# Kernel tuning notes

Hardware: AMD Instinct MI355X
Metric: run time of the kernel (lower is better)

Reference implementation:

```python
import jax, jax.numpy as jnp
import numpy as np


def _rope_tables(N, d, base=10000.0):
    # LLaMA-style: freqs over even dims, interleaved (pairs) layout
    inv = 1.0 / (base ** (np.arange(0, d, 2)[: d // 2].astype(np.float32) / d))
    ang = np.outer(np.arange(N, dtype=np.float32), inv)  # [N, d/2]
    return jnp.asarray(np.cos(ang), jnp.float32), jnp.asarray(np.sin(ang), jnp.float32)


def _apply_rope(x, cos, sin):
    # x: [B, h, N, d]; pairs layout (..., d/2, 2)
    B, h, N, d = x.shape
    xs = x.reshape(B, h, N, d // 2, 2)
    x0, x1 = xs[..., 0], xs[..., 1]
    c = cos[None, None, :, :]
    s = sin[None, None, :, :]
    o0 = x0 * c - x1 * s
    o1 = x1 * c + x0 * s
    return jnp.stack([o0, o1], axis=-1).reshape(B, h, N, d)


def _neighborhood_attn(q, k, v, window, scale):
    # q,k,v: [B, h, H, W, d]; NATTEN-style clamped window of size window x window
    B, h, H, W, d = q.shape
    r = window // 2
    ih = jnp.clip(jnp.arange(H) - r, 0, H - window)[:, None] + jnp.arange(window)  # [H, w]
    iw = jnp.clip(jnp.arange(W) - r, 0, W - window)[:, None] + jnp.arange(window)  # [W, w]
    # gather windows: [B, h, H, W, w, w, d]
    kwin = k[:, :, ih[:, None, :, None], iw[None, :, None, :], :]
    vwin = v[:, :, ih[:, None, :, None], iw[None, :, None, :], :]
    attn = jnp.einsum('bhijd,bhijpqd->bhijpq', q, kwin) * scale
    attn = jax.nn.softmax(attn.reshape(B, h, H, W, window * window), axis=-1)
    out = jnp.einsum('bhijp,bhijpd->bhijd', attn,
                     vwin.reshape(B, h, H, W, window * window, d))
    return out  # [B, h, H, W, d]


def setup_inputs() -> dict:
    key = jax.random.key(0)
    k1, k2, k3 = jax.random.split(key, 3)
    B, H, W, C = 2, 56, 56, 256
    N = H * W
    x = jax.random.normal(k1, (B, N, C), dtype=jnp.float32)
    Wqkv = jax.random.normal(k2, (C, 3 * C), dtype=jnp.float32) * 0.02
    Wproj = jax.random.normal(k3, (C, C), dtype=jnp.float32) * 0.02
    bproj = jnp.zeros((C,), dtype=jnp.float32)
    return {"x": x, "Wqkv": Wqkv, "Wproj": Wproj, "bproj": bproj, "H": H, "W": W}


def reference(x, Wqkv, Wproj, bproj, H, W):
    head_dim = 32
    window = 7
    B, N, C = x.shape
    heads = C // head_dim
    scale = head_dim ** (-0.5)

    qkv = (x @ Wqkv).reshape(B, N, 3, heads, head_dim)
    qkv = jnp.transpose(qkv, (2, 0, 3, 1, 4))  # [3, B, h, N, d]
    q, k, v = qkv[0], qkv[1], qkv[2]

    cos, sin = _rope_tables(N, head_dim)
    q = _apply_rope(q, cos, sin)
    k = _apply_rope(k, cos, sin)

    q = q.reshape(B, heads, H, W, head_dim)
    k = k.reshape(B, heads, H, W, head_dim)
    v = v.reshape(B, heads, H, W, head_dim)

    out = _neighborhood_attn(q, k, v, window, scale)  # [B, h, H, W, d]
    out = out.reshape(B, heads, N, head_dim)
    out = jnp.transpose(out, (0, 2, 1, 3)).reshape(B, N, C)
    return out @ Wproj + bproj
```

## Files before the change

kernel.cpp:

```cpp
#include <hip/hip_runtime.h>
#include <hip/hip_bf16.h>

#define HH 56
#define WW 56
#define NPOS 3136
#define BATCH 2
#define HEADS 8

typedef __attribute__((ext_vector_type(4))) float floatx4;
typedef __attribute__((ext_vector_type(8))) short short8;
typedef __attribute__((ext_vector_type(2))) _Float16 half2v;

static __device__ __forceinline__ ushort f2b(float f) {
    __hip_bfloat16 h = __float2bfloat16(f);
    return *reinterpret_cast<ushort*>(&h);
}
static __device__ __forceinline__ float b2f(ushort u) {
    return __uint_as_float(((uint)u) << 16);
}
static __device__ __forceinline__ ushort f2h(float f) {
    union { _Float16 h; ushort u; } c; c.h = (_Float16)f; return c.u;
}
static __device__ __forceinline__ half2v u2h2(uint u) {
    union { uint u; half2v h; } c; c.u = u; return c.h;
}

static __device__ __forceinline__ void async16(const ushort* g, ushort* l) {
    __builtin_amdgcn_global_load_lds(
        (const __attribute__((address_space(1))) unsigned int*)g,
        (__attribute__((address_space(3))) unsigned int*)l, 16, 0, 0);
}

__constant__ float INVF[16] = {
    1.0f,   0.5623413251903491f,   0.31622776601683794f,   0.17782794100389228f,
    0.1f,   0.05623413251903491f,  0.031622776601683794f,  0.017782794100389228f,
    0.01f,  0.005623413251903491f, 0.0031622776601683794f, 0.0017782794100389228f,
    0.001f, 0.0005623413251903491f,0.00031622776601683794f,0.00017782794100389228f
};

#define QSCALE 0.17677669529663687f


__global__ __launch_bounds__(256) void prep(
    const float* __restrict__ wqkv, const float* __restrict__ wproj,
    ushort* __restrict__ wqkvT, ushort* __restrict__ wprojT)
{
    __shared__ ushort Ls[64 * 65];
    const int bid = blockIdx.x, t = threadIdx.x;
    if (bid < 48) {
        int nb = (bid % 12) * 64, kb = (bid / 12) * 64;
#pragma unroll
        for (int i = 0; i < 16; ++i) {
            int e = t + 256 * i, kk = e >> 6, nn = e & 63;
            Ls[kk * 65 + nn] = f2b(wqkv[(size_t)(kb + kk) * 768 + nb + nn]);
        }
        __syncthreads();
#pragma unroll
        for (int i = 0; i < 16; ++i) {
            int e = t + 256 * i, nn = e >> 6, kk = e & 63;
            wqkvT[(size_t)(nb + nn) * 256 + kb + kk] = Ls[kk * 65 + nn];
        }
    } else {
        int l = bid - 48;
        int nb = (l & 3) * 64, kb = (l >> 2) * 64;
#pragma unroll
        for (int i = 0; i < 16; ++i) {
            int e = t + 256 * i, kk = e >> 6, nn = e & 63;
            Ls[kk * 65 + nn] = f2b(wproj[(size_t)(kb + kk) * 256 + nb + nn]);
        }
        __syncthreads();
#pragma unroll
        for (int i = 0; i < 16; ++i) {
            int e = t + 256 * i, nn = e >> 6, kk = e & 63;
            wprojT[(size_t)(nb + nn) * 256 + kb + kk] = Ls[kk * 65 + nn];
        }
    }
}

__global__ __launch_bounds__(256) void qkv_fast(
    const float* __restrict__ x, const ushort* __restrict__ wqkvT,
    ushort* __restrict__ qb, ushort* __restrict__ kws, ushort* __restrict__ vws)
{
    __shared__ ushort Ab[128 * 32];
    __shared__ ushort Bb[128 * 32];
    const int t = threadIdx.x;
    const int lane = t & 63, wv = t >> 6;
    const int qm = lane & 15, quad = lane >> 4;
    const int m0 = blockIdx.y * 128, n0 = blockIdx.x * 128;
    const int wr = wv >> 1, wc = wv & 1;
    const int srow = lane >> 2, scol = (lane & 3) * 8;
    const int arow = t >> 1, aseg = (t & 1) * 16;

    floatx4 acc[4][4];
#pragma unroll
    for (int i = 0; i < 4; ++i)
#pragma unroll
        for (int j = 0; j < 4; ++j) acc[i][j] = (floatx4){0.f, 0.f, 0.f, 0.f};

    for (int k0 = 0; k0 < 256; k0 += 32) {
#pragma unroll
        for (int i = 0; i < 4; ++i) {
            int col = aseg + i * 4;
            float4 v = *(const float4*)&x[(size_t)(m0 + arow) * 256 + k0 + col];
            ushort4 h; h.x = f2b(v.x); h.y = f2b(v.y); h.z = f2b(v.z); h.w = f2b(v.w);
            *(ushort4*)&Ab[arow * 32 + col] = h;
        }
#pragma unroll
        for (int j = 0; j < 2; ++j) {
            int rbase = wv * 32 + j * 16;
            async16(&wqkvT[(size_t)(n0 + rbase + srow) * 256 + k0 + scol], &Bb[rbase * 32]);
        }
        __syncthreads();
        short8 af[4], bf[4];
#pragma unroll
        for (int mt = 0; mt < 4; ++mt)
            af[mt] = *(const short8*)&Ab[(wr * 64 + mt * 16 + qm) * 32 + quad * 8];
#pragma unroll
        for (int nt = 0; nt < 4; ++nt)
            bf[nt] = *(const short8*)&Bb[(wc * 64 + nt * 16 + qm) * 32 + quad * 8];
#pragma unroll
        for (int mt = 0; mt < 4; ++mt)
#pragma unroll
            for (int nt = 0; nt < 4; ++nt)
                acc[mt][nt] = __builtin_amdgcn_mfma_f32_16x16x32_bf16(af[mt], bf[nt], acc[mt][nt], 0, 0, 0);
        __syncthreads();
    }

    const int whichB = n0 >> 8;
#pragma unroll
    for (int mt = 0; mt < 4; ++mt) {
#pragma unroll
        for (int r = 0; r < 4; ++r) {
            int m = m0 + wr * 64 + mt * 16 + quad * 4 + r;
            int b = (m >= NPOS) ? 1 : 0;
            int pos = m - b * NPOS;
            float c0 = 0.f, s0 = 0.f, c1 = 0.f, s1 = 0.f;
            if (whichB < 2) {
                float posf = (float)pos;
                __sincosf(posf * INVF[qm >> 1], &s0, &c0);
                __sincosf(posf * INVF[8 + (qm >> 1)], &s1, &c1);
            }
#pragma unroll
            for (int nt = 0; nt < 4; ++nt) {
                int c = n0 + wc * 64 + nt * 16 + qm;
                int head = (c >> 5) & 7;
                int d = (nt & 1) * 16 + qm;
                float val = acc[mt][nt][r];
                if (whichB < 2) {
                    float other = __shfl_xor(val, 1);
                    float cf = (nt & 1) ? c1 : c0, sf = (nt & 1) ? s1 : s0;
                    val = (lane & 1) ? (val * cf + other * sf)
                                     : (val * cf - other * sf);
                }
                if (whichB == 0) {
                    qb[(size_t)m * 256 + head * 32 + d] = f2h(val * QSCALE);
                } else {
                    ushort* dst = (whichB == 1) ? kws : vws;
                    dst[(size_t)(((b << 3) + head) * NPOS + pos) * 32 + d] = f2h(val);
                }
            }
        }
    }
}

__global__ __launch_bounds__(256) void nattn(
    const ushort* __restrict__ kws, const ushort* __restrict__ vws,
    const ushort* __restrict__ qb, ushort* __restrict__ ab)
{
    __shared__ ushort Ksm[196 * 32];
    __shared__ ushort Vsm[196 * 32];
    const int t = threadIdx.x;
    const int bh = blockIdx.y;
    const int b = bh >> 3, head = bh & 7;
    const int ti = blockIdx.x / 7, tj = blockIdx.x % 7;
    const int ty0 = ti * 8, tx0 = tj * 8;
    const int r0 = min(max(ty0 - 3, 0), HH - 14);
    const int c0 = min(max(tx0 - 3, 0), WW - 14);
    const ushort* kbase = kws + (size_t)bh * NPOS * 32;
    const ushort* vbase = vws + (size_t)bh * NPOS * 32;

    for (int idx = t; idx < 196 * 4; idx += 256) {
        int p = idx >> 2, ch = idx & 3;
        int g = ((r0 + p / 14) * WW + (c0 + p % 14)) * 32 + ch * 8;
        *(uint4*)&Ksm[p * 32 + ch * 8] = *(const uint4*)&kbase[g];
        *(uint4*)&Vsm[p * 32 + ch * 8] = *(const uint4*)&vbase[g];
    }
    __syncthreads();

    const int lane = t & 63, wv = t >> 6;
    const int qsub = lane & 15, part = lane >> 4;
    const int qi = wv * 16 + qsub;
    const int qy = ty0 + (qi >> 3), qx = tx0 + (qi & 7);
    const int pos = qy * WW + qx;
    const size_t qoff = (size_t)(b * NPOS + pos) * 256 + head * 32;

    half2v qp[16];
    {
        const uint* q4 = (const uint*)(qb + qoff);
#pragma unroll
        for (int c2 = 0; c2 < 16; ++c2) qp[c2] = u2h2(q4[c2]);
    }

    const int rs = min(max(qy - 3, 0), HH - 7) - r0;
    const int cs = min(max(qx - 3, 0), WW - 7) - c0;

    float sum = 0.f;
    float facc[32];
#pragma unroll
    for (int c = 0; c < 32; ++c) facc[c] = 0.f;

#pragma unroll
    for (int j = 0; j < 13; ++j) {
        int kk = part + 4 * j;
        if (kk < 49) {
            int kp = (rs + kk / 7) * 14 + (cs + kk % 7);
            const uint4* Kp = (const uint4*)&Ksm[kp * 32];
            float s = 0.f;
#pragma unroll
            for (int c8 = 0; c8 < 4; ++c8) {
                uint4 u = Kp[c8];
#if __has_builtin(__builtin_amdgcn_fdot2)
                s = __builtin_amdgcn_fdot2(u2h2(u.x), qp[4 * c8 + 0], s, false);
                s = __builtin_amdgcn_fdot2(u2h2(u.y), qp[4 * c8 + 1], s, false);
                s = __builtin_amdgcn_fdot2(u2h2(u.z), qp[4 * c8 + 2], s, false);
                s = __builtin_amdgcn_fdot2(u2h2(u.w), qp[4 * c8 + 3], s, false);
#else
                half2v k0h = u2h2(u.x), k1h = u2h2(u.y), k2h = u2h2(u.z), k3h = u2h2(u.w);
                half2v q0 = qp[4 * c8 + 0], q1 = qp[4 * c8 + 1];
                half2v q2 = qp[4 * c8 + 2], q3 = qp[4 * c8 + 3];
                s += (float)k0h[0] * (float)q0[0] + (float)k0h[1] * (float)q0[1];
                s += (float)k1h[0] * (float)q1[0] + (float)k1h[1] * (float)q1[1];
                s += (float)k2h[0] * (float)q2[0] + (float)k2h[1] * (float)q2[1];
                s += (float)k3h[0] * (float)q3[0] + (float)k3h[1] * (float)q3[1];
#endif
            }
            float e = __expf(s);
            sum += e;
            const uint4* Vp = (const uint4*)&Vsm[kp * 32];
#pragma unroll
            for (int c8 = 0; c8 < 4; ++c8) {
                uint4 u = Vp[c8];
                float* fv = facc + 8 * c8;
                half2v h0 = u2h2(u.x), h1 = u2h2(u.y), h2 = u2h2(u.z), h3 = u2h2(u.w);
                fv[0] += e * (float)h0[0]; fv[1] += e * (float)h0[1];
                fv[2] += e * (float)h1[0]; fv[3] += e * (float)h1[1];
                fv[4] += e * (float)h2[0]; fv[5] += e * (float)h2[1];
                fv[6] += e * (float)h3[0]; fv[7] += e * (float)h3[1];
            }
        }
    }
    sum += __shfl_xor(sum, 16);
    sum += __shfl_xor(sum, 32);
#pragma unroll
    for (int c = 0; c < 32; ++c) {
        facc[c] += __shfl_xor(facc[c], 16);
        facc[c] += __shfl_xor(facc[c], 32);
    }

    if (part == 0) {
        float inv = 1.f / sum;
        uint* op = (uint*)(ab + qoff);
#pragma unroll
        for (int c2 = 0; c2 < 16; ++c2) {
            uint lo = f2b(facc[2 * c2] * inv);
            uint hi = f2b(facc[2 * c2 + 1] * inv);
            op[c2] = lo | (hi << 16);
        }
    }
}

__global__ __launch_bounds__(256) void proj_fast(
    const ushort* __restrict__ ab, const ushort* __restrict__ wprojT,
    const float* __restrict__ bias, float* __restrict__ out)
{
    __shared__ ushort Ap[64 * 32];
    __shared__ ushort Bp[64 * 32];
    const int t = threadIdx.x;
    const int lane = t & 63, wv = t >> 6;
    const int qm = lane & 15, quad = lane >> 4;
    const int n0 = blockIdx.x * 64, m0 = blockIdx.y * 64;
    const int wr = wv >> 1, wc = wv & 1;
    const int srow = lane >> 2, scol = (lane & 3) * 8;

    floatx4 acc[2][2];
#pragma unroll
    for (int i = 0; i < 2; ++i)
#pragma unroll
        for (int j = 0; j < 2; ++j) acc[i][j] = (floatx4){0.f, 0.f, 0.f, 0.f};

    for (int k0 = 0; k0 < 256; k0 += 32) {
        int rbase = wv * 16;
        async16(&ab[(size_t)(m0 + rbase + srow) * 256 + k0 + scol], &Ap[rbase * 32]);
        async16(&wprojT[(size_t)(n0 + rbase + srow) * 256 + k0 + scol], &Bp[rbase * 32]);
        __syncthreads();
        short8 af[2], bf[2];
#pragma unroll
        for (int mt = 0; mt < 2; ++mt)
            af[mt] = *(const short8*)&Ap[(wr * 32 + mt * 16 + qm) * 32 + quad * 8];
#pragma unroll
        for (int nt = 0; nt < 2; ++nt)
            bf[nt] = *(const short8*)&Bp[(wc * 32 + nt * 16 + qm) * 32 + quad * 8];
#pragma unroll
        for (int mt = 0; mt < 2; ++mt)
#pragma unroll
            for (int nt = 0; nt < 2; ++nt)
                acc[mt][nt] = __builtin_amdgcn_mfma_f32_16x16x32_bf16(af[mt], bf[nt], acc[mt][nt], 0, 0, 0);
        __syncthreads();
    }

#pragma unroll
    for (int nt = 0; nt < 2; ++nt) {
        int c = n0 + wc * 32 + nt * 16 + qm;
        float bv = bias[c];
#pragma unroll
        for (int mt = 0; mt < 2; ++mt) {
#pragma unroll
            for (int r = 0; r < 4; ++r) {
                int m = m0 + wr * 32 + mt * 16 + quad * 4 + r;
                out[(size_t)m * 256 + c] = acc[mt][nt][r] + bv;
            }
        }
    }
}

__global__ __launch_bounds__(256) void qkv_fb(
    const float* __restrict__ x, const float* __restrict__ w,
    float* __restrict__ qa, ushort* __restrict__ kws, ushort* __restrict__ vws)
{
    __shared__ ushort Asm[64 * 40];
    __shared__ ushort Bsm[64 * 40];
    const int t = threadIdx.x;
    const int m0 = blockIdx.y * 64;
    const int n0 = blockIdx.x * 64;
    const int lane = t & 63, wv = t >> 6;
    const int qm = lane & 15, quad = lane >> 4;

    floatx4 acc[4];
#pragma unroll
    for (int i = 0; i < 4; ++i) acc[i] = (floatx4){0.f, 0.f, 0.f, 0.f};

    for (int k0 = 0; k0 < 256; k0 += 32) {
#pragma unroll
        for (int i = 0; i < 2; ++i) {
            int p = t + 256 * i;
            int row = p >> 3, f4 = p & 7;
            float4 v = *(const float4*)&x[(size_t)(m0 + row) * 256 + k0 + f4 * 4];
            ushort4 h;
            h.x = f2b(v.x); h.y = f2b(v.y); h.z = f2b(v.z); h.w = f2b(v.w);
            *(ushort4*)&Asm[row * 40 + f4 * 4] = h;
        }
#pragma unroll
        for (int i = 0; i < 8; ++i) {
            int e = t + 256 * i;
            int kk = e >> 6, nn = e & 63;
            Bsm[nn * 40 + kk] = f2b(w[(size_t)(k0 + kk) * 768 + n0 + nn]);
        }
        __syncthreads();
        short8 af = *(const short8*)&Asm[(wv * 16 + qm) * 40 + quad * 8];
#pragma unroll
        for (int nt = 0; nt < 4; ++nt) {
            short8 bf = *(const short8*)&Bsm[(nt * 16 + qm) * 40 + quad * 8];
            acc[nt] = __builtin_amdgcn_mfma_f32_16x16x32_bf16(af, bf, acc[nt], 0, 0, 0);
        }
        __syncthreads();
    }

    const int whichB = n0 >> 8;
#pragma unroll
    for (int r = 0; r < 4; ++r) {
        int m = m0 + wv * 16 + quad * 4 + r;
        int b = (m >= NPOS) ? 1 : 0;
        int pos = m - b * NPOS;
        float cf[2], sf[2];
        if (whichB < 2) {
            float posf = (float)pos;
            __sincosf(posf * INVF[qm >> 1], &sf[0], &cf[0]);
            __sincosf(posf * INVF[8 + (qm >> 1)], &sf[1], &cf[1]);
        }
#pragma unroll
        for (int nt = 0; nt < 4; ++nt) {
            int par = nt & 1;
            int d = par * 16 + qm;
            int head = ((n0 >> 5) & 7) + (nt >> 1);
            float val = acc[nt][r];
            if (whichB < 2) {
                float other = __shfl_xor(val, 1);
                val = (lane & 1) ? (val * cf[par] + other * sf[par])
                                 : (val * cf[par] - other * sf[par]);
            }
            if (whichB == 0) {
                qa[(size_t)m * 256 + head * 32 + d] = val;
            } else {
                ushort* dst = (whichB == 1) ? kws : vws;
                dst[(size_t)(((b << 3) + head) * NPOS + pos) * 32 + d] = f2b(val);
            }
        }
    }
}

__global__ __launch_bounds__(256) void nattn_fb(
    const ushort* __restrict__ kws, const ushort* __restrict__ vws, float* qa)
{
    __shared__ ushort Ksm[196 * 32];
    __shared__ ushort Vsm[196 * 32];
    const int t = threadIdx.x;
    const int bh = blockIdx.y;
    const int b = bh >> 3, head = bh & 7;
    const int ti = blockIdx.x / 7, tj = blockIdx.x % 7;
    const int ty0 = ti * 8, tx0 = tj * 8;
    const int r0 = min(max(ty0 - 3, 0), HH - 14);
    const int c0 = min(max(tx0 - 3, 0), WW - 14);
    const ushort* kbase = kws + (size_t)bh * NPOS * 32;
    const ushort* vbase = vws + (size_t)bh * NPOS * 32;

    for (int idx = t; idx < 196 * 4; idx += 256) {
        int p = idx >> 2, ch = idx & 3;
        int g = ((r0 + p / 14) * WW + (c0 + p % 14)) * 32 + ch * 8;
        *(uint4*)&Ksm[p * 32 + ch * 8] = *(const uint4*)&kbase[g];
        *(uint4*)&Vsm[p * 32 + ch * 8] = *(const uint4*)&vbase[g];
    }
    __syncthreads();

    const int lane = t & 63, wv = t >> 6;
    const int qsub = lane & 15, part = lane >> 4;
    const int qi = wv * 16 + qsub;
    const int qy = ty0 + (qi >> 3), qx = tx0 + (qi & 7);
    const int pos = qy * WW + qx;
    float* qptr = qa + (size_t)(b * NPOS + pos) * 256 + head * 32;

    float qf[32];
#pragma unroll
    for (int c4 = 0; c4 < 8; ++c4) {
        float4 v = *(const float4*)&qptr[c4 * 4];
        qf[4 * c4] = v.x; qf[4 * c4 + 1] = v.y; qf[4 * c4 + 2] = v.z; qf[4 * c4 + 3] = v.w;
    }

    const int rs = min(max(qy - 3, 0), HH - 7) - r0;
    const int cs = min(max(qx - 3, 0), WW - 7) - c0;

    float sum = 0.f;
    float facc[32];
#pragma unroll
    for (int c = 0; c < 32; ++c) facc[c] = 0.f;
#pragma unroll
    for (int j = 0; j < 13; ++j) {
        int kk = part + 4 * j;
        if (kk < 49) {
            int kp = (rs + kk / 7) * 14 + (cs + kk % 7);
            const uint4* Kp = (const uint4*)&Ksm[kp * 32];
            float s = 0.f;
#pragma unroll
            for (int c8 = 0; c8 < 4; ++c8) {
                uint4 u = Kp[c8];
                const float* qv = qf + 8 * c8;
                s += qv[0] * b2f((ushort)u.x) + qv[1] * b2f((ushort)(u.x >> 16));
                s += qv[2] * b2f((ushort)u.y) + qv[3] * b2f((ushort)(u.y >> 16));
                s += qv[4] * b2f((ushort)u.z) + qv[5] * b2f((ushort)(u.z >> 16));
                s += qv[6] * b2f((ushort)u.w) + qv[7] * b2f((ushort)(u.w >> 16));
            }
            float e = __expf(s * 0.17677669529663687f);
            sum += e;
            const uint4* Vp = (const uint4*)&Vsm[kp * 32];
#pragma unroll
            for (int c8 = 0; c8 < 4; ++c8) {
                uint4 u = Vp[c8];
                float* fv = facc + 8 * c8;
                fv[0] += e * b2f((ushort)u.x); fv[1] += e * b2f((ushort)(u.x >> 16));
                fv[2] += e * b2f((ushort)u.y); fv[3] += e * b2f((ushort)(u.y >> 16));
                fv[4] += e * b2f((ushort)u.z); fv[5] += e * b2f((ushort)(u.z >> 16));
                fv[6] += e * b2f((ushort)u.w); fv[7] += e * b2f((ushort)(u.w >> 16));
            }
        }
    }
    sum += __shfl_xor(sum, 16);
    sum += __shfl_xor(sum, 32);
#pragma unroll
    for (int c = 0; c < 32; ++c) {
        facc[c] += __shfl_xor(facc[c], 16);
        facc[c] += __shfl_xor(facc[c], 32);
    }

    if (part == 0) {
        float inv = 1.f / sum;
#pragma unroll
        for (int c4 = 0; c4 < 8; ++c4) {
            float4 o;
            o.x = facc[4 * c4] * inv; o.y = facc[4 * c4 + 1] * inv;
            o.z = facc[4 * c4 + 2] * inv; o.w = facc[4 * c4 + 3] * inv;
            *(float4*)&qptr[c4 * 4] = o;
        }
    }
}

__global__ __launch_bounds__(256) void proj_fb(
    const float* __restrict__ w, const float* __restrict__ bias, float* out)
{
    __shared__ ushort Apad[64 * 264];
    __shared__ ushort Bsm[256 * 40];
    const int t = threadIdx.x;
    const int m0 = blockIdx.x * 64;
    const int lane = t & 63, wv = t >> 6;
    const int qm = lane & 15, quad = lane >> 4;

    {
        int row = t >> 2, cb = (t & 3) * 64;
        const float4* src = (const float4*)&out[(size_t)(m0 + row) * 256 + cb];
#pragma unroll
        for (int i = 0; i < 16; ++i) {
            float4 v = src[i];
            ushort4 h;
            h.x = f2b(v.x); h.y = f2b(v.y); h.z = f2b(v.z); h.w = f2b(v.w);
            *(ushort4*)&Apad[row * 264 + cb + i * 4] = h;
        }
    }

    floatx4 acc[4][4];
#pragma unroll
    for (int i = 0; i < 4; ++i)
#pragma unroll
        for (int j = 0; j < 4; ++j) acc[i][j] = (floatx4){0.f, 0.f, 0.f, 0.f};

    __syncthreads();

    for (int k0 = 0; k0 < 256; k0 += 32) {
#pragma unroll
        for (int i = 0; i < 32; ++i) {
            int e = t + 256 * i;
            int kk = e >> 8, nn = e & 255;
            Bsm[nn * 40 + kk] = f2b(w[(size_t)(k0 + kk) * 256 + nn]);
        }
        __syncthreads();
        short8 af[4];
#pragma unroll
        for (int mt = 0; mt < 4; ++mt)
            af[mt] = *(const short8*)&Apad[(mt * 16 + qm) * 264 + k0 + quad * 8];
#pragma unroll
        for (int nt = 0; nt < 4; ++nt) {
            short8 bf = *(const short8*)&Bsm[(wv * 64 + nt * 16 + qm) * 40 + quad * 8];
#pragma unroll
            for (int mt = 0; mt < 4; ++mt)
                acc[mt][nt] = __builtin_amdgcn_mfma_f32_16x16x32_bf16(af[mt], bf, acc[mt][nt], 0, 0, 0);
        }
        __syncthreads();
    }

#pragma unroll
    for (int nt = 0; nt < 4; ++nt) {
        int c = wv * 64 + nt * 16 + qm;
        float bv = bias[c];
#pragma unroll
        for (int mt = 0; mt < 4; ++mt) {
#pragma unroll
            for (int r = 0; r < 4; ++r) {
                int m = m0 + mt * 16 + quad * 4 + r;
                out[(size_t)m * 256 + c] = acc[mt][nt][r] + bv;
            }
        }
    }
}

extern "C" void kernel_launch(void* const* d_in, const int* in_sizes, int n_in,
                              void* d_out, int out_size, void* d_ws, size_t ws_size,
                              hipStream_t stream)
{
    const float* x     = (const float*)d_in[0];
    const float* wqkv  = (const float*)d_in[1];
    const float* wproj = (const float*)d_in[2];
    const float* bproj = (const float*)d_in[3];
    float* out = (float*)d_out;
    char* ws = (char*)d_ws;

    if (ws_size >= 13369344ull) {
        ushort* wqkvT  = (ushort*)(ws);
        ushort* wprojT = (ushort*)(ws + 393216);
        ushort* qb     = (ushort*)(ws + 524288);
        ushort* kws    = (ushort*)(ws + 3735552);
        ushort* vws    = (ushort*)(ws + 6946816);
        ushort* ab     = (ushort*)(ws + 10158080);

        hipLaunchKernelGGL(prep, dim3(64), dim3(256), 0, stream,
                           wqkv, wproj, wqkvT, wprojT);
        hipLaunchKernelGGL(qkv_fast, dim3(6, 49), dim3(256), 0, stream,
                           x, wqkvT, qb, kws, vws);
        hipLaunchKernelGGL(nattn, dim3(49, BATCH * HEADS), dim3(256), 0, stream,
                           kws, vws, qb, ab);
        hipLaunchKernelGGL(proj_fast, dim3(4, 98), dim3(256), 0, stream,
                           ab, wprojT, bproj, out);
    } else {
        ushort* kws = (ushort*)ws;
        ushort* vws = (ushort*)(ws + 3211264);
        hipLaunchKernelGGL(qkv_fb, dim3(12, 98), dim3(256), 0, stream,
                           x, wqkv, out, kws, vws);
        hipLaunchKernelGGL(nattn_fb, dim3(49, BATCH * HEADS), dim3(256), 0, stream,
                           kws, vws, out);
        hipLaunchKernelGGL(proj_fb, dim3(98), dim3(256), 0, stream,
                           wproj, bproj, out);
    }
}
```

Measured before the change: 115.3 us.

## Pre-convert x to bf16 in prep, async-load A tiles, fp16 PV accumulation

The prep kernel now also converts the fp32 input x to a bf16 workspace copy. The QKV GEMM can then load its A tiles with async global-to-LDS loads, like the B tiles, instead of converting from fp32 in registers, and it reads half the bytes per tile. Separately, the neighborhood attention accumulates the probability-weighted V sum in packed fp16 vectors rather than fp32 scalars, halving the multiply-add count. This adds a separate conversion pass over x and lowers accumulation precision, which risks fp16 rounding error in the attention output.

Measured after the change: 110.9 us, median of 2. 3.8% less time.

```diff
diff --git a/kernel.cpp b/kernel.cpp
--- a/kernel.cpp
+++ b/kernel.cpp
@@ -42,13 +42,24 @@
 
 
 __global__ __launch_bounds__(256) void prep(
+    const float* __restrict__ x,
     const float* __restrict__ wqkv, const float* __restrict__ wproj,
-    ushort* __restrict__ wqkvT, ushort* __restrict__ wprojT)
+    ushort* __restrict__ xb, ushort* __restrict__ wqkvT,
+    ushort* __restrict__ wprojT)
 {
     __shared__ ushort Ls[64 * 65];
     const int bid = blockIdx.x, t = threadIdx.x;
-    if (bid < 48) {
-        int nb = (bid % 12) * 64, kb = (bid / 12) * 64;
+    if (bid < 98) {
+#pragma unroll
+        for (int i = 0; i < 16; ++i) {
+            int idx4 = bid * 4096 + i * 256 + t;
+            float4 v = *(const float4*)&x[(size_t)idx4 * 4];
+            ushort4 h; h.x = f2b(v.x); h.y = f2b(v.y); h.z = f2b(v.z); h.w = f2b(v.w);
+            *(ushort4*)&xb[(size_t)idx4 * 4] = h;
+        }
+    } else if (bid < 146) {
+        int l = bid - 98;
+        int nb = (l % 12) * 64, kb = (l / 12) * 64;
 #pragma unroll
         for (int i = 0; i < 16; ++i) {
             int e = t + 256 * i, kk = e >> 6, nn = e & 63;
@@ -61,7 +72,7 @@
             wqkvT[(size_t)(nb + nn) * 256 + kb + kk] = Ls[kk * 65 + nn];
         }
     } else {
-        int l = bid - 48;
+        int l = bid - 146;
         int nb = (l & 3) * 64, kb = (l >> 2) * 64;
 #pragma unroll
         for (int i = 0; i < 16; ++i) {
@@ -78,7 +89,7 @@
 }
 
 __global__ __launch_bounds__(256) void qkv_fast(
-    const float* __restrict__ x, const ushort* __restrict__ wqkvT,
+    const ushort* __restrict__ xb, const ushort* __restrict__ wqkvT,
     ushort* __restrict__ qb, ushort* __restrict__ kws, ushort* __restrict__ vws)
 {
     __shared__ ushort Ab[128 * 32];
@@ -89,7 +100,6 @@
     const int m0 = blockIdx.y * 128, n0 = blockIdx.x * 128;
     const int wr = wv >> 1, wc = wv & 1;
     const int srow = lane >> 2, scol = (lane & 3) * 8;
-    const int arow = t >> 1, aseg = (t & 1) * 16;
 
     floatx4 acc[4][4];
 #pragma unroll
@@ -98,16 +108,10 @@
         for (int j = 0; j < 4; ++j) acc[i][j] = (floatx4){0.f, 0.f, 0.f, 0.f};
 
     for (int k0 = 0; k0 < 256; k0 += 32) {
-#pragma unroll
-        for (int i = 0; i < 4; ++i) {
-            int col = aseg + i * 4;
-            float4 v = *(const float4*)&x[(size_t)(m0 + arow) * 256 + k0 + col];
-            ushort4 h; h.x = f2b(v.x); h.y = f2b(v.y); h.z = f2b(v.z); h.w = f2b(v.w);
-            *(ushort4*)&Ab[arow * 32 + col] = h;
-        }
 #pragma unroll
         for (int j = 0; j < 2; ++j) {
             int rbase = wv * 32 + j * 16;
+            async16(&xb[(size_t)(m0 + rbase + srow) * 256 + k0 + scol], &Ab[rbase * 32]);
             async16(&wqkvT[(size_t)(n0 + rbase + srow) * 256 + k0 + scol], &Bb[rbase * 32]);
         }
         __syncthreads();
@@ -205,9 +209,9 @@
     const int cs = min(max(qx - 3, 0), WW - 7) - c0;
 
     float sum = 0.f;
-    float facc[32];
-#pragma unroll
-    for (int c = 0; c < 32; ++c) facc[c] = 0.f;
+    half2v vacc[16];
+#pragma unroll
+    for (int c = 0; c < 16; ++c) vacc[c] = (half2v){(_Float16)0.f, (_Float16)0.f};
 
 #pragma unroll
     for (int j = 0; j < 13; ++j) {
@@ -236,21 +240,28 @@
             }
             float e = __expf(s);
             sum += e;
+            _Float16 eh = (_Float16)e;
+            half2v e2 = (half2v){eh, eh};
             const uint4* Vp = (const uint4*)&Vsm[kp * 32];
 #pragma unroll
             for (int c8 = 0; c8 < 4; ++c8) {
                 uint4 u = Vp[c8];
-                float* fv = facc + 8 * c8;
-                half2v h0 = u2h2(u.x), h1 = u2h2(u.y), h2 = u2h2(u.z), h3 = u2h2(u.w);
-                fv[0] += e * (float)h0[0]; fv[1] += e * (float)h0[1];
-                fv[2] += e * (float)h1[0]; fv[3] += e * (float)h1[1];
-                fv[4] += e * (float)h2[0]; fv[5] += e * (float)h2[1];
-                fv[6] += e * (float)h3[0]; fv[7] += e * (float)h3[1];
+                vacc[4 * c8 + 0] += e2 * u2h2(u.x);
+                vacc[4 * c8 + 1] += e2 * u2h2(u.y);
+                vacc[4 * c8 + 2] += e2 * u2h2(u.z);
+                vacc[4 * c8 + 3] += e2 * u2h2(u.w);
             }
         }
     }
     sum += __shfl_xor(sum, 16);
     sum += __shfl_xor(sum, 32);
+
+    float facc[32];
+#pragma unroll
+    for (int c2 = 0; c2 < 16; ++c2) {
+        facc[2 * c2]     = (float)vacc[c2][0];
+        facc[2 * c2 + 1] = (float)vacc[c2][1];
+    }
 #pragma unroll
     for (int c = 0; c < 32; ++c) {
         facc[c] += __shfl_xor(facc[c], 16);
@@ -570,18 +581,19 @@
     float* out = (float*)d_out;
     char* ws = (char*)d_ws;
 
-    if (ws_size >= 13369344ull) {
+    if (ws_size >= 16580608ull) {
         ushort* wqkvT  = (ushort*)(ws);
         ushort* wprojT = (ushort*)(ws + 393216);
-        ushort* qb     = (ushort*)(ws + 524288);
-        ushort* kws    = (ushort*)(ws + 3735552);
-        ushort* vws    = (ushort*)(ws + 6946816);
-        ushort* ab     = (ushort*)(ws + 10158080);
-
-        hipLaunchKernelGGL(prep, dim3(64), dim3(256), 0, stream,
-                           wqkv, wproj, wqkvT, wprojT);
+        ushort* xb     = (ushort*)(ws + 524288);
+        ushort* qb     = (ushort*)(ws + 3735552);
+        ushort* kws    = (ushort*)(ws + 6946816);
+        ushort* vws    = (ushort*)(ws + 10158080);
+        ushort* ab     = (ushort*)(ws + 13369344);
+
+        hipLaunchKernelGGL(prep, dim3(162), dim3(256), 0, stream,
+                           x, wqkv, wproj, xb, wqkvT, wprojT);
         hipLaunchKernelGGL(qkv_fast, dim3(6, 49), dim3(256), 0, stream,
-                           x, wqkvT, qb, kws, vws);
+                           xb, wqkvT, qb, kws, vws);
         hipLaunchKernelGGL(nattn, dim3(49, BATCH * HEADS), dim3(256), 0, stream,
                            kws, vws, qb, ab);
         hipLaunchKernelGGL(proj_fast, dim3(4, 98), dim3(256), 0, stream,
```
